# Optimization experiments

Measured on AMD Instinct MI355X. Metric: run time of the kernel, lower is better.

The kernel has to match this reference:

```python
import jax, jax.numpy as jnp
import numpy as np
from jax import lax

# 4th-order Butterworth lowpass, scipy.signal.butter(4, 0.2)
B_COEF = np.array([0.004824343357716228, 0.019297373430864913, 0.02894606014629737,
                   0.019297373430864913, 0.004824343357716228], dtype=np.float32)
A_COEF = np.array([1.0, -2.369513007182038, 2.3139884144006453,
                   -1.0546654058785672, 0.18737949236818502], dtype=np.float32)


def setup_inputs() -> dict:
    key = jax.random.key(0)
    x = jax.random.normal(key, (8, 64, 48000), dtype=jnp.float32)
    return {"x": x, "b": jnp.asarray(B_COEF), "a": jnp.asarray(A_COEF)}


def _pad_odd(x, n):
    # Faithful to torch _pad_odd (including its exact slicing on the right side).
    left = 2.0 * x[..., 0:1] - jnp.flip(x[..., 0:n], axis=-1)
    right = 2.0 * x[..., -1:] - jnp.flip(x[..., -(n + 2):-2], axis=-1)
    return jnp.concatenate([left, x, right], axis=-1)


def _lfilter(x, a, b):
    # y[n] = (sum_k b[k] x[n-k] - sum_j a[j] y[n-j]) / a[0]
    a0 = a[0]
    bn = b / a0
    an = a[1:] / a0                      # [N], N = order
    ntaps = b.shape[0]                   # static
    N = a.shape[0] - 1                   # static
    T = x.shape[-1]
    # FIR part: small static tap loop, fully vectorized over batch/time.
    pad = [(0, 0)] * (x.ndim - 1) + [(ntaps - 1, 0)]
    xp = jnp.pad(x, pad)
    f = bn[0] * xp[..., ntaps - 1: ntaps - 1 + T]
    for k in range(1, ntaps):
        f = f + bn[k] * xp[..., ntaps - 1 - k: ntaps - 1 - k + T]
    # IIR recurrence via scan over time.
    f_t = jnp.moveaxis(f, -1, 0)         # [T, B, C]
    init = jnp.zeros(x.shape[:-1] + (N,), x.dtype)  # [B, C, N], y[t-1..t-N]

    def step(carry, ft):
        y = ft - jnp.einsum('k,...k->...', an, carry)
        carry = jnp.concatenate([y[..., None], carry[..., :-1]], axis=-1)
        return carry, y

    _, ys = lax.scan(step, init, f_t)
    return jnp.moveaxis(ys, 0, -1)       # [B, C, T]


def _filtfilt(x, a, b):
    y = _lfilter(x, a, b)
    return jnp.flip(_lfilter(jnp.flip(y, axis=-1), a, b), axis=-1)


def reference(x, b, a):
    scale = jnp.max(jnp.abs(x), axis=-1, keepdims=True)
    xs = x / scale
    padlen = 3 * max(int(a.shape[0]), int(b.shape[0]))  # 15, static
    xp = _pad_odd(xs, padlen)
    y = _filtfilt(xp, a, b)
    y = y[..., padlen:-padlen]
    return y * scale
```

## Files before the change

kernel.cpp:

```cpp
#include <hip/hip_runtime.h>


#define T48   48000
#define TP0   48030
#define LCH   48
#define NCH   1024
#define SECF  12288
#define OSEC  12000
#define UF    12560

__global__ __launch_bounds__(1024, 4) void filtfilt_k(
    const float* __restrict__ x, const float* __restrict__ bco,
    const float* __restrict__ aco, float* __restrict__ out)
{
  __shared__ __align__(16) float U[UF];
  __shared__ float P[10][16];

  const int c = threadIdx.x;
  const float* __restrict__ xs = x + (size_t)blockIdx.x * T48;
  float* __restrict__ os = out + (size_t)blockIdx.x * T48;

  const float inva0 = 1.f / aco[0];
  const float b0 = bco[0]*inva0, b1 = bco[1]*inva0, b2 = bco[2]*inva0,
              b3 = bco[3]*inva0, b4 = bco[4]*inva0;
  const float na1 = -aco[1]*inva0, na2 = -aco[2]*inva0,
              na3 = -aco[3]*inva0, na4 = -aco[4]*inva0;

  if (c < 64) {
    const int i = (c >> 2) & 3, j = c & 3;
    float r1 = (j==0)?1.f:0.f, r2 = (j==1)?1.f:0.f,
          r3 = (j==2)?1.f:0.f, r4 = (j==3)?1.f:0.f;
#pragma unroll
    for (int n = 0; n < LCH; n++) {
      float h = fmaf(na1, r1, fmaf(na2, r2, fmaf(na3, r3, na4 * r4)));
      r4 = r3; r3 = r2; r2 = r1; r1 = h;
    }
    float c0 = __shfl(r1, j), c1 = __shfl(r2, j),
          c2 = __shfl(r3, j), c3 = __shfl(r4, j);
    float Pv = (i==0)?c0 : (i==1)?c1 : (i==2)?c2 : c3;
    if (c < 16) P[0][c] = Pv;
#pragma unroll
    for (int k = 0; k < 9; k++) {
      float rA0 = __shfl(Pv, i*4+0), rA1 = __shfl(Pv, i*4+1),
            rA2 = __shfl(Pv, i*4+2), rA3 = __shfl(Pv, i*4+3);
      float cB0 = __shfl(Pv, 0*4+j), cB1 = __shfl(Pv, 1*4+j),
            cB2 = __shfl(Pv, 2*4+j), cB3 = __shfl(Pv, 3*4+j);
      Pv = rA0*cB0 + rA1*cB1 + rA2*cB2 + rA3*cB3;
      if (c < 16) P[k+1][c] = Pv;
    }
  }

  float A[LCH];
  float w1 = 0.f, w2 = 0.f, w3 = 0.f, w4 = 0.f;
  for (int s = 0; s < 4; s++) {
    __syncthreads();
    const int p0 = SECF * s;
#pragma unroll
    for (int j = 0; j < 13; j++) {
      int i = 1024*j + c;
      if (i < SECF + 4) {
        int p = p0 - 4 + i;
        int q = p - 15;
        float v = 0.f;
        if (q >= 0 && q < T48)               v = xs[q];
        else if (p >= 0 && p < 15)           v = 2.f*xs[0] - xs[14 - p];
        else if (p >= T48+15 && p < TP0)     v = 2.f*xs[T48-1] - xs[2*T48 + 12 - p];
        U[i + i/48] = v;
      }
    }
    __syncthreads();
    if ((c >> 8) == s) {
      const int cl = c & 255;
      const int rb = 49 * cl;
      w4 = U[rb+0]; w3 = U[rb+1]; w2 = U[rb+2]; w1 = U[rb+3];
#pragma unroll
      for (int n = 0; n < LCH; n++) A[n] = U[rb + (n+4) + ((n+4) >> 6 >= 0 ? (n+4)/48 : 0)];
    }
  }
  __syncthreads();

  float r1 = 0.f, r2 = 0.f, r3 = 0.f, r4 = 0.f;
#pragma unroll
  for (int n = 0; n < LCH; n++) {
    float xv = A[n];
    float f = fmaf(b0,xv, fmaf(b1,w1, fmaf(b2,w2, fmaf(b3,w3, b4*w4))));
    w4 = w3; w3 = w2; w2 = w1; w1 = xv;
    float u = fmaf(na4, r4, f);
    u = fmaf(na3, r3, u); u = fmaf(na2, r2, u); u = fmaf(na1, r1, u);
    A[n] = u; r4 = r3; r3 = r2; r2 = r1; r1 = u;
  }

  float4* Sb0 = (float4*)U;
  float4* Sb1 = (float4*)U + 1024;
  Sb0[c] = make_float4(r1, r2, r3, r4);
  __syncthreads();
#pragma unroll
  for (int k = 0; k < 10; k++) {
    float4* cur = (k & 1) ? Sb1 : Sb0;
    float4* nxt = (k & 1) ? Sb0 : Sb1;
    const int off = 1 << k;
    float4 t = cur[c];
    if (c >= off) {
      float4 q = cur[c - off];
      t.x += P[k][0]*q.x  + P[k][1]*q.y  + P[k][2]*q.z  + P[k][3]*q.w;
      t.y += P[k][4]*q.x  + P[k][5]*q.y  + P[k][6]*q.z  + P[k][7]*q.w;
      t.z += P[k][8]*q.x  + P[k][9]*q.y  + P[k][10]*q.z + P[k][11]*q.w;
      t.w += P[k][12]*q.x + P[k][13]*q.y + P[k][14]*q.z + P[k][15]*q.w;
    }
    nxt[c] = t;
    __syncthreads();
  }
  float4 sv = make_float4(0.f,0.f,0.f,0.f);
  if (c > 0) sv = Sb0[c-1];

  {
    float h1 = sv.x, h2 = sv.y, h3 = sv.z, h4 = sv.w;
#pragma unroll
    for (int n = 0; n < LCH; n++) {
      float h = fmaf(na1, h1, fmaf(na2, h2, fmaf(na3, h3, na4 * h4)));
      A[n] += h;
      h4 = h3; h3 = h2; h2 = h1; h1 = h;
    }
  }
  if (c >= 1000) {
#pragma unroll
    for (int n = 0; n < LCH; n++) if (48*c + n >= TP0) A[n] = 0.f;
  }

  Sb1[c] = make_float4(A[0], A[1], A[2], A[3]);
  __syncthreads();
  float h0 = 0.f, h1v = 0.f, h2v = 0.f, h3v = 0.f;
  if (c < NCH - 1) { float4 hv = Sb1[c+1]; h0 = hv.x; h1v = hv.y; h2v = hv.z; h3v = hv.w; }

#define YV(i) ((i) < 48 ? A[(i)] : ((i)==48 ? h0 : (i)==49 ? h1v : (i)==50 ? h2v : h3v))
  r1 = 0.f; r2 = 0.f; r3 = 0.f; r4 = 0.f;
#pragma unroll
  for (int m = 0; m < LCH; m++) {
    float g = fmaf(b0, YV(47-m), fmaf(b1, YV(48-m),
              fmaf(b2, YV(49-m), fmaf(b3, YV(50-m), b4 * YV(51-m)))));
    float u = fmaf(na4, r4, g);
    u = fmaf(na3, r3, u); u = fmaf(na2, r2, u); u = fmaf(na1, r1, u);
    r4 = r3; r3 = r2; r2 = r1; r1 = u;
    if      (m == 0) h3v = u;
    else if (m == 1) h2v = u;
    else if (m == 2) h1v = u;
    else if (m == 3) h0  = u;
    else             A[51 - m] = u;
  }
#undef YV

  const int d = NCH - 1 - c;
  Sb0[d] = make_float4(r1, r2, r3, r4);
  __syncthreads();
#pragma unroll
  for (int k = 0; k < 10; k++) {
    float4* cur = (k & 1) ? Sb1 : Sb0;
    float4* nxt = (k & 1) ? Sb0 : Sb1;
    const int off = 1 << k;
    float4 t = cur[d];
    if (d >= off) {
      float4 q = cur[d - off];
      t.x += P[k][0]*q.x  + P[k][1]*q.y  + P[k][2]*q.z  + P[k][3]*q.w;
      t.y += P[k][4]*q.x  + P[k][5]*q.y  + P[k][6]*q.z  + P[k][7]*q.w;
      t.z += P[k][8]*q.x  + P[k][9]*q.y  + P[k][10]*q.z + P[k][11]*q.w;
      t.w += P[k][12]*q.x + P[k][13]*q.y + P[k][14]*q.z + P[k][15]*q.w;
    }
    nxt[d] = t;
    __syncthreads();
  }
  float4 ev = make_float4(0.f,0.f,0.f,0.f);
  if (d > 0) ev = Sb0[d-1];

  {
    float g1 = ev.x, g2 = ev.y, g3 = ev.z, g4 = ev.w;
#pragma unroll
    for (int m = 0; m < LCH; m++) {
      float h = fmaf(na1, g1, fmaf(na2, g2, fmaf(na3, g3, na4 * g4)));
      if      (m == 0) h3v += h;
      else if (m == 1) h2v += h;
      else if (m == 2) h1v += h;
      else if (m == 3) h0  += h;
      else             A[51 - m] += h;
      g4 = g3; g3 = g2; g2 = g1; g1 = h;
    }
  }

  __syncthreads();
  const int tb = 48*c - 15;
  const int sA = (tb < 0 ? 0 : tb / OSEC);
  const int sB = (tb + 47) / OSEC;
  for (int s = 0; s < 4; s++) {
    const int t0 = OSEC * s;
    if (s == sA || s == sB) {
      const int RL49 = 49 * (c - 250*s);
      const int ibase = tb - t0;
#pragma unroll
      for (int k = 0; k < 48; k++) {
        int i = ibase + k;
        if ((unsigned)i < (unsigned)OSEC) {
          float v = (k < 44) ? A[k+4]
                  : (k == 44) ? h0 : (k == 45) ? h1v : (k == 46) ? h2v : h3v;
          U[RL49 + k - 15 - (k < 15 ? 1 : 0)] = v;
        }
      }
    }
    __syncthreads();
#pragma unroll
    for (int j = 0; j < 12; j++) {
      int i = 1024*j + c;
      if (i < OSEC) os[t0 + i] = U[i + i/48];
    }
    __syncthreads();
  }
}

extern "C" void kernel_launch(void* const* d_in, const int* in_sizes, int n_in,
                              void* d_out, int out_size, void* d_ws, size_t ws_size,
                              hipStream_t stream) {
  (void)n_in; (void)d_ws; (void)ws_size; (void)out_size;
  const float* x = (const float*)d_in[0];
  const float* b = (const float*)d_in[1];
  const float* a = (const float*)d_in[2];
  float* out = (float*)d_out;
  const int nseq = in_sizes[0] / T48;
  filtfilt_k<<<dim3(nseq), dim3(1024), 0, stream>>>(x, b, a, out);
}
```

Baseline: 207.1 us.

## Vectorize global loads/stores to float4 and prefetch next input section into registers

Replaces scalar global reads of the padded input with float4 loads, prefetching the next section into registers while the current section is staged in LDS, so global latency overlaps with the shared-memory transpose. The LDS staging layout changes to float4 granularity with a padding of one float4 per 12, and threads read their 48-sample chunk as 14 float4s. The output path likewise writes float4s to global memory, gathering shifted elements out of LDS because of the 15-sample pad offset. It adds register pressure from the prefetch buffer and more complex index math.

Result: no change. 204.6 us (-1.2%).

```diff
diff --git a/kernel.cpp b/kernel.cpp
--- a/kernel.cpp
+++ b/kernel.cpp
@@ -1,13 +1,15 @@
 #include <hip/hip_runtime.h>
 
 
-#define T48   48000
-#define TP0   48030
-#define LCH   48
-#define NCH   1024
-#define SECF  12288
-#define OSEC  12000
-#define UF    12560
+#define T48 48000
+#define TP0 48030
+#define LCH 48
+#define NCH 1024
+#define UF  13344
+
+__device__ __forceinline__ float fget(const float4& v, int e) {
+  switch (e & 3) { case 0: return v.x; case 1: return v.y; case 2: return v.z; default: return v.w; }
+}
 
 __global__ __launch_bounds__(1024, 4) void filtfilt_k(
     const float* __restrict__ x, const float* __restrict__ bco,
@@ -18,13 +20,23 @@
 
   const int c = threadIdx.x;
   const float* __restrict__ xs = x + (size_t)blockIdx.x * T48;
+  const float4* __restrict__ xs4 = reinterpret_cast<const float4*>(xs);
   float* __restrict__ os = out + (size_t)blockIdx.x * T48;
+  float4* __restrict__ os4 = reinterpret_cast<float4*>(os);
+  float4* __restrict__ U4 = reinterpret_cast<float4*>(U);
 
   const float inva0 = 1.f / aco[0];
   const float b0 = bco[0]*inva0, b1 = bco[1]*inva0, b2 = bco[2]*inva0,
               b3 = bco[3]*inva0, b4 = bco[4]*inva0;
   const float na1 = -aco[1]*inva0, na2 = -aco[2]*inva0,
               na3 = -aco[3]*inva0, na4 = -aco[4]*inva0;
+
+  float4 R[4];
+#pragma unroll
+  for (int j = 0; j < 4; j++) {
+    int g = 1024*j + c;
+    if (g < 3074) { int m = min(max(g - 5, 0), 11999); R[j] = xs4[m]; }
+  }
 
   if (c < 64) {
     const int i = (c >> 2) & 3, j = c & 3;
@@ -50,31 +62,48 @@
     }
   }
 
+  float w4v, w3v, w2v, w1v;
   float A[LCH];
-  float w1 = 0.f, w2 = 0.f, w3 = 0.f, w4 = 0.f;
   for (int s = 0; s < 4; s++) {
     __syncthreads();
-    const int p0 = SECF * s;
-#pragma unroll
-    for (int j = 0; j < 13; j++) {
-      int i = 1024*j + c;
-      if (i < SECF + 4) {
-        int p = p0 - 4 + i;
-        int q = p - 15;
-        float v = 0.f;
-        if (q >= 0 && q < T48)               v = xs[q];
-        else if (p >= 0 && p < 15)           v = 2.f*xs[0] - xs[14 - p];
-        else if (p >= T48+15 && p < TP0)     v = 2.f*xs[T48-1] - xs[2*T48 + 12 - p];
-        U[i + i/48] = v;
+#pragma unroll
+    for (int j = 0; j < 4; j++) {
+      int g = 1024*j + c;
+      if (g < 3074) {
+        float4 v = R[j];
+        bool slow = (s == 0 && g <= 4) || (s == 3 && g >= 2789);
+        if (slow) {
+          float x0d = 2.f * xs[0], xld = 2.f * xs[T48-1];
+#pragma unroll
+          for (int e = 0; e < 4; e++) {
+            int p = 12288*s - 5 + 4*g + e;
+            float vv = 0.f;
+            if (s == 0) { if (p >= 0) vv = x0d - xs[14 - p]; }
+            else        { if (p < TP0) vv = xld - xs[96012 - p]; }
+            if (e == 0) v.x = vv; else if (e == 1) v.y = vv;
+            else if (e == 2) v.z = vv; else v.w = vv;
+          }
+        }
+        U4[g + g/12] = v;
+      }
+    }
+    if (s < 3) {
+#pragma unroll
+      for (int j = 0; j < 4; j++) {
+        int g = 1024*j + c;
+        if (g < 3074) { int m = min(max(3072*(s+1) - 5 + g, 0), 11999); R[j] = xs4[m]; }
       }
     }
     __syncthreads();
     if ((c >> 8) == s) {
       const int cl = c & 255;
-      const int rb = 49 * cl;
-      w4 = U[rb+0]; w3 = U[rb+1]; w2 = U[rb+2]; w1 = U[rb+3];
-#pragma unroll
-      for (int n = 0; n < LCH; n++) A[n] = U[rb + (n+4) + ((n+4) >> 6 >= 0 ? (n+4)/48 : 0)];
+      float4 F[14];
+#pragma unroll
+      for (int k = 0; k < 14; k++)
+        F[k] = U4[13*cl + k + (k >= 12 ? 1 : 0)];
+      w4v = F[0].y; w3v = F[0].z; w2v = F[0].w; w1v = F[1].x;
+#pragma unroll
+      for (int n = 0; n < LCH; n++) A[n] = fget(F[(n + 5) >> 2], (n + 5) & 3);
     }
   }
   __syncthreads();
@@ -83,15 +112,15 @@
 #pragma unroll
   for (int n = 0; n < LCH; n++) {
     float xv = A[n];
-    float f = fmaf(b0,xv, fmaf(b1,w1, fmaf(b2,w2, fmaf(b3,w3, b4*w4))));
-    w4 = w3; w3 = w2; w2 = w1; w1 = xv;
+    float f = fmaf(b0,xv, fmaf(b1,w1v, fmaf(b2,w2v, fmaf(b3,w3v, b4*w4v))));
+    w4v = w3v; w3v = w2v; w2v = w1v; w1v = xv;
     float u = fmaf(na4, r4, f);
     u = fmaf(na3, r3, u); u = fmaf(na2, r2, u); u = fmaf(na1, r1, u);
     A[n] = u; r4 = r3; r3 = r2; r2 = r1; r1 = u;
   }
 
-  float4* Sb0 = (float4*)U;
-  float4* Sb1 = (float4*)U + 1024;
+  float4* Sb0 = U4;
+  float4* Sb1 = U4 + 1024;
   Sb0[c] = make_float4(r1, r2, r3, r4);
   __syncthreads();
 #pragma unroll
@@ -186,29 +215,30 @@
   }
 
   __syncthreads();
-  const int tb = 48*c - 15;
-  const int sA = (tb < 0 ? 0 : tb / OSEC);
-  const int sB = (tb + 47) / OSEC;
   for (int s = 0; s < 4; s++) {
-    const int t0 = OSEC * s;
-    if (s == sA || s == sB) {
-      const int RL49 = 49 * (c - 250*s);
-      const int ibase = tb - t0;
-#pragma unroll
-      for (int k = 0; k < 48; k++) {
-        int i = ibase + k;
-        if ((unsigned)i < (unsigned)OSEC) {
-          float v = (k < 44) ? A[k+4]
-                  : (k == 44) ? h0 : (k == 45) ? h1v : (k == 46) ? h2v : h3v;
-          U[RL49 + k - 15 - (k < 15 ? 1 : 0)] = v;
-        }
-      }
-    }
-    __syncthreads();
-#pragma unroll
-    for (int j = 0; j < 12; j++) {
-      int i = 1024*j + c;
-      if (i < OSEC) os[t0 + i] = U[i + i/48];
+#pragma unroll
+    for (int k4 = 0; k4 < 12; k4++) {
+      int u4 = 12*c - 3 + k4;
+      unsigned lu4 = (unsigned)(u4 - 3000*s);
+      if (lu4 <= 3000u) {
+        float4 v;
+        if (k4 < 11) v = make_float4(A[4*k4+4], A[4*k4+5], A[4*k4+6], A[4*k4+7]);
+        else         v = make_float4(h0, h1v, h2v, h3v);
+        U4[(int)lu4 + (int)lu4/12] = v;
+      }
+    }
+    __syncthreads();
+#pragma unroll
+    for (int j = 0; j < 3; j++) {
+      int t4l = 1024*j + c;
+      if (t4l < 3000) {
+        int q0 = t4l, q1 = t4l + 1;
+        int a0 = 4*(q0 + q0/12) + 3;
+        int bi = 4*(q1 + q1/12);
+        float4 v;
+        v.x = U[a0]; v.y = U[bi]; v.z = U[bi+1]; v.w = U[bi+2];
+        os4[3000*s + t4l] = v;
+      }
     }
     __syncthreads();
   }
```
